# Optimization experiments

Hardware: AMD Instinct MI355X
Metric: run time of the kernel (lower is better)

## Reference

```python
import jax, jax.numpy as jnp
import numpy as np

DT = 0.05      # bsde.delta_t
EPS = 1e-6     # BatchNormalization epsilon


def _bn(x, gamma, beta):
    # training-mode batch norm: statistics over the batch axis
    m = jnp.mean(x, axis=0, keepdims=True)
    v = jnp.var(x, axis=0, keepdims=True)
    return (x - m) * jax.lax.rsqrt(v + EPS) * gamma + beta


def _subnet(x, g0, b0, W0, g1, b1, W1, g2, b2, W2, bias2, g3, b3):
    # bn -> (dense -> bn -> relu) x 2 -> dense(+bias) -> bn
    x = _bn(x, g0, b0)
    x = jax.nn.relu(_bn(x @ W0, g1, b1))
    x = jax.nn.relu(_bn(x @ W1, g2, b2))
    x = _bn(x @ W2 + bias2, g3, b3)
    return x


def setup_inputs() -> dict:
    key = jax.random.key(0)
    B, D, N, H = 8192, 100, 20, 110
    T = N - 1  # number of subnets
    ks = jax.random.split(key, 18)
    u = lambda k, s, lo, hi: jax.random.uniform(k, s, jnp.float32, lo, hi)
    s_dh = np.sqrt(2.0 / (D + H)).astype(np.float32)
    s_hh = np.sqrt(2.0 / (H + H)).astype(np.float32)
    s_hd = np.sqrt(2.0 / (H + D)).astype(np.float32)
    return {
        "dw": jax.random.normal(ks[0], (B, D, N), jnp.float32) * np.sqrt(DT).astype(np.float32),
        "x": jax.random.normal(ks[1], (B, D, N + 1), jnp.float32),
        "mean_y_input": jax.random.normal(ks[2], (N,), jnp.float32),
        "y_init": u(ks[3], (1,), 0.0, 1.0),
        "z_init": u(ks[4], (1, D), -0.1, 0.1),
        "gamma0": u(ks[5], (T, D), 0.1, 0.5),
        "beta0": 0.1 * jax.random.normal(ks[6], (T, D), jnp.float32),
        "W0": s_dh * jax.random.normal(ks[7], (T, D, H), jnp.float32),
        "gamma1": u(ks[8], (T, H), 0.1, 0.5),
        "beta1": 0.1 * jax.random.normal(ks[9], (T, H), jnp.float32),
        "W1": s_hh * jax.random.normal(ks[10], (T, H, H), jnp.float32),
        "gamma2": u(ks[11], (T, H), 0.1, 0.5),
        "beta2": 0.1 * jax.random.normal(ks[12], (T, H), jnp.float32),
        "W2": s_hd * jax.random.normal(ks[13], (T, H, D), jnp.float32),
        "bias2": jnp.zeros((T, D), jnp.float32),
        "gamma3": u(ks[14], (T, D), 0.1, 0.5),
        "beta3": 0.1 * jax.random.normal(ks[15], (T, D), jnp.float32),
    }


def reference(dw, x, mean_y_input, y_init, z_init, gamma0, beta0, W0,
              gamma1, beta1, W1, gamma2, beta2, W2, bias2, gamma3, beta3):
    B, D, N = dw.shape
    T = N - 1
    # z at step t+1 depends only on x[:, :, t+1] and subnet t -> compute all in parallel
    x_steps = jnp.moveaxis(x[:, :, 1:N], 2, 0)  # [T, B, D]
    z_all = jax.vmap(_subnet)(x_steps, gamma0, beta0, W0, gamma1, beta1, W1,
                              gamma2, beta2, W2, bias2, gamma3, beta3) / D  # [T, B, D]
    z0 = jnp.broadcast_to(z_init, (B, D))          # all_one_vec @ z_init
    zs = jnp.concatenate([z0[None], z_all], axis=0)  # [N, B, D] (z used at each update)
    dw_steps = jnp.moveaxis(dw, 2, 0)               # [N, B, D]
    y0 = jnp.ones((B, 1), dw.dtype) * y_init

    def step(y, zd):
        z, dwt = zd
        # f_tf(t, x, y, z) = sin(y) for the SineBM equation
        y_new = y - DT * jnp.sin(y) + jnp.sum(z * dwt, axis=1, keepdims=True)
        return y_new, jnp.mean(y_new)

    y_final, means = jax.lax.scan(step, y0, (zs, dw_steps))
    mean_y = jnp.concatenate([jnp.mean(y0)[None], means[:T]])  # length N
    return y_final, mean_y
```

## Files before the change

kernel.cpp:

```cpp
#include <hip/hip_runtime.h>

typedef unsigned short u16;
typedef unsigned int   u32;

#define BATCH  8192
#define DIM    100
#define HID    110
#define TSUB   19
#define NSTEP  20
#define KP     128
#define NPAD   112
#define BN_EPS 1e-6f
#define DT_C   0.05f

#define SAB  2048
#define SAR  (BATCH / SAB)
#define SLICES 32
#define NBLK_SCAN 2048
#define NMT  64

typedef __bf16 v8bf __attribute__((ext_vector_type(8)));
typedef float  v4f  __attribute__((ext_vector_type(4)));
typedef float  v2f  __attribute__((ext_vector_type(2)));
typedef u16    u16x4 __attribute__((ext_vector_type(4)));

__device__ __forceinline__ u16 f2bf(float f) {
    u32 u = __float_as_uint(f);
    return (u16)((u + 0x7fffu + ((u >> 16) & 1u)) >> 16);
}
__device__ __forceinline__ float bf2f(u16 h) {
    return __uint_as_float(((u32)h) << 16);
}
__device__ __forceinline__ void acc4(float4& s, float4& q, float4 v) {
    s.x += v.x; s.y += v.y; s.z += v.z; s.w += v.w;
    q.x += v.x * v.x; q.y += v.y * v.y; q.z += v.z * v.z; q.w += v.w * v.w;
}

__global__ void statsA(const float* __restrict__ x, float* __restrict__ part,
                       u32* __restrict__ xT32) {
    __shared__ u16 xls[SAR][2112];
    const int tid = threadIdx.x;
    const int b0 = blockIdx.x * SAR;
    float4 s0 = {0,0,0,0}, q0 = {0,0,0,0};
    float4 s1 = {0,0,0,0}, q1 = {0,0,0,0};
    float4 s2 = {0,0,0,0}, q2 = {0,0,0,0};
#pragma unroll
    for (int r = 0; r < SAR; r++) {
        const float4* row = (const float4*)(x + (size_t)(b0 + r) * 2100);
        float4 v0 = row[tid];
        float4 v1 = row[tid + 256];
        acc4(s0, q0, v0);
        acc4(s1, q1, v1);
        u16x4 p0 = { f2bf(v0.x), f2bf(v0.y), f2bf(v0.z), f2bf(v0.w) };
        u16x4 p1 = { f2bf(v1.x), f2bf(v1.y), f2bf(v1.z), f2bf(v1.w) };
        *(u16x4*)&xls[r][tid * 4]        = p0;
        *(u16x4*)&xls[r][1024 + tid * 4] = p1;
        if (tid < 13) {
            float4 v2 = row[tid + 512];
            acc4(s2, q2, v2);
            u16x4 p2 = { f2bf(v2.x), f2bf(v2.y), f2bf(v2.z), f2bf(v2.w) };
            *(u16x4*)&xls[r][2048 + tid * 4] = p2;
        }
    }
    float* ps = part + (size_t)blockIdx.x * 4200;
    *(float4*)&ps[tid * 4]               = s0;
    *(float4*)&ps[1024 + tid * 4]        = s1;
    *(float4*)&ps[2100 + tid * 4]        = q0;
    *(float4*)&ps[2100 + 1024 + tid * 4] = q1;
    if (tid < 13) {
        *(float4*)&ps[2048 + tid * 4]        = s2;
        *(float4*)&ps[2100 + 2048 + tid * 4] = q2;
    }
    __syncthreads();
    const int TOT = TSUB * SAR * (NPAD / 2);
    for (int i = tid; i < TOT; i += 256) {
        int w = i % (NPAD / 2);
        int seg = i / (NPAD / 2);
        int r = seg % SAR, t = seg / SAR;
        int d0 = w * 2;
        u32 v = 0;
        if (d0 < DIM) {
            u16 lo = xls[r][d0 * 21 + t + 1];
            u16 hi = (d0 + 1 < DIM) ? xls[r][(d0 + 1) * 21 + t + 1] : (u16)0;
            v = (u32)lo | ((u32)hi << 16);
        }
        xT32[((size_t)t * BATCH + b0 + r) * (NPAD / 2) + w] = v;
    }
}

__global__ void statsB(const float* __restrict__ part, float* __restrict__ slpart) {
    int gid = blockIdx.x * 256 + threadIdx.x;
    if (gid >= 4200 * SLICES) return;
    int slice = gid / 4200;
    int o = gid - slice * 4200;
    const float* p = part + (size_t)slice * (SAB / SLICES) * 4200 + o;
    float acc = 0.f;
#pragma unroll 8
    for (int i = 0; i < SAB / SLICES; i++) acc += p[(size_t)i * 4200];
    slpart[(size_t)slice * 4200 + o] = acc;
}

__global__ void statsC(const float* __restrict__ slpart, float* __restrict__ sum0) {
    int o = blockIdx.x * 256 + threadIdx.x;
    if (o >= 4200) return;
    float s = 0.f;
#pragma unroll
    for (int i = 0; i < SLICES; i++) s += slpart[(size_t)i * 4200 + o];
    sum0[o] = s;
}

__global__ void wtrans(const float* __restrict__ W0, const float* __restrict__ W1,
                       const float* __restrict__ W2, u16* __restrict__ WTsw) {
    __shared__ float lw[HID * HID];
    const int t = blockIdx.x, l = blockIdx.y, tid = threadIdx.x;
    const float* W; int K, N;
    if (l == 0)      { W = W0; K = DIM; N = HID; }
    else if (l == 1) { W = W1; K = HID; N = HID; }
    else             { W = W2; K = HID; N = DIM; }
    const float* Wt = W + (size_t)t * K * N;
    for (int i = tid; i < K * N; i += 256) lw[i] = Wt[i];
    __syncthreads();
    u16* out = WTsw + ((size_t)l * TSUB + t) * (NPAD * KP);
    for (int i = tid; i < NPAD * 16; i += 256) {
        int n = i / 16, p = i % 16;
        int kc = p ^ (n & 7);
        u16 o8[8];
#pragma unroll
        for (int j = 0; j < 8; j++) {
            int k = kc * 8 + j;
            float v = (k < K && n < N) ? lw[k * N + n] : 0.f;
            o8[j] = f2bf(v);
        }
        *(uint4*)&out[(size_t)n * KP + p * 8] = *(uint4*)o8;
    }
}

__global__ void scaleW0(const float* __restrict__ sum0, const float* __restrict__ sq0,
                        const float* __restrict__ g0, u16* __restrict__ WT0) {
    __shared__ float aL[DIM];
    const int t = blockIdx.x, tid = threadIdx.x;
    if (tid < DIM) {
        int idx = tid * 21 + (t + 1);
        float m = sum0[idx] * (1.f / BATCH);
        float v = sq0[idx] * (1.f / BATCH) - m * m;
        aL[tid] = g0[t * DIM + tid] * rsqrtf(v + BN_EPS);
    }
    __syncthreads();
    u16* wt = WT0 + (size_t)t * NPAD * KP;
    for (int i = tid; i < NPAD * 16; i += 256) {
        int n = i >> 4, p = i & 15;
        int kc = p ^ (n & 7);
        uint4 v4 = *(uint4*)&wt[(size_t)n * KP + p * 8];
        u16* e = (u16*)&v4;
#pragma unroll
        for (int j = 0; j < 8; j++) {
            int k = kc * 8 + j;
            if (k < DIM) e[j] = f2bf(bf2f(e[j]) * aL[k]);
        }
        *(uint4*)&wt[(size_t)n * KP + p * 8] = v4;
    }
}

template <int KREAL, int NOUT, int AFFINE, int RELU, int BMAJOR>
__global__ __launch_bounds__(512, 4)
void gemm_kernel(const u16* __restrict__ Ain,
                 const u16* __restrict__ WTswL,
                 const float* __restrict__ partIn,
                 const float* __restrict__ gIn,
                 const float* __restrict__ bIn,
                 u16* __restrict__ Hout,
                 float* __restrict__ partOut) {
    __shared__ __align__(16) u16 Blds[NPAD * KP];
    __shared__ float s_sum[NPAD], s_sq[NPAD];
    __shared__ float aAffL[KP], cAffL[KP];

    const int tid = threadIdx.x;
    const int mt = blockIdx.x;
    const int t  = blockIdx.y;
    const int brow0 = mt * 128;

    if (tid < NPAD) { s_sum[tid] = 0.f; s_sq[tid] = 0.f; }
    if (AFFINE) {
        if (tid >= KREAL && tid < KP) { aAffL[tid] = 0.f; cAffL[tid] = 0.f; }
        if (tid < KREAL) {
            float s = 0.f, q = 0.f;
#pragma unroll 8
            for (int m2 = 0; m2 < NMT; m2++) {
                const float* pp = partIn + ((size_t)(m2 * TSUB + t) * 2) * NPAD;
                s += pp[tid];
                q += pp[NPAD + tid];
            }
            float m = s * (1.f / BATCH);
            float v = q * (1.f / BATCH) - m * m;
            float rstd = rsqrtf(v + BN_EPS);
            int idx = t * KREAL + tid;
            float ga = gIn[idx] * rstd;
            aAffL[tid] = ga;
            cAffL[tid] = bIn[idx] - m * ga;
        }
    }

    {
        const uint4* wsrc = (const uint4*)(WTswL + (size_t)t * NPAD * KP);
        uint4* bl = (uint4*)Blds;
        for (int i = tid; i < NPAD * KP / 8; i += 512) bl[i] = wsrc[i];
    }
    __syncthreads();

    const int lane = tid & 63;
    const int wv   = tid >> 6;
    const int r0   = lane & 15;
    const int q    = lane >> 4;
    const int row  = wv * 16 + r0;

    const u16* arow = Ain + ((size_t)t * BATCH + brow0 + row) * NPAD;
    u16 hv[4][8];
#pragma unroll
    for (int ks = 0; ks < 4; ks++) {
        int cb = ks * 4 + q;
        int cbl = (cb > 13) ? 13 : cb;
        *(uint4*)hv[ks] = *(const uint4*)(arow + cbl * 8);
    }
    v8bf afr[4];
#pragma unroll
    for (int ks = 0; ks < 4; ks++) {
        if (AFFINE) {
            int cb = ks * 4 + q;
            const float* ap = &aAffL[cb * 8];
            const float* cp = &cAffL[cb * 8];
            u16 pk[8];
#pragma unroll
            for (int j = 0; j < 8; j++) {
                float av = fmaf(bf2f(hv[ks][j]), ap[j], cp[j]);
                if (RELU) av = fmaxf(av, 0.f);
                pk[j] = f2bf(av);
            }
            afr[ks] = *(v8bf*)pk;
        } else {
            afr[ks] = *(v8bf*)hv[ks];
        }
    }

    v4f acc[7];
#pragma unroll
    for (int j = 0; j < 7; j++) { v4f z = {0.f, 0.f, 0.f, 0.f}; acc[j] = z; }
#pragma unroll
    for (int ks = 0; ks < 4; ks++) {
        int cbase = ks * 4 + q;
#pragma unroll
        for (int nf = 0; nf < 7; nf++) {
            int nr = nf * 16 + r0;
            v8bf bfr = *(const v8bf*)&Blds[nr * KP + ((cbase ^ (nr & 7)) * 8)];
            acc[nf] = __builtin_amdgcn_mfma_f32_16x16x32_bf16(afr[ks], bfr, acc[nf], 0, 0, 0);
        }
    }

#pragma unroll
    for (int nf = 0; nf < 7; nf++) {
        int n = nf * 16 + r0;
#pragma unroll
        for (int rg = 0; rg < 4; rg++) {
            int grow = brow0 + wv * 16 + q * 4 + rg;
            size_t oidx = BMAJOR ? ((size_t)grow * (TSUB * NPAD) + (size_t)t * NPAD + n)
                                 : (((size_t)t * BATCH + grow) * NPAD + n);
            Hout[oidx] = f2bf(acc[nf][rg]);
        }
    }
#pragma unroll
    for (int nf = 0; nf < 7; nf++) {
        float cs = 0.f, cq = 0.f;
#pragma unroll
        for (int rg = 0; rg < 4; rg++) {
            float vv = acc[nf][rg];
            cs += vv; cq += vv * vv;
        }
        cs += __shfl_xor(cs, 16); cs += __shfl_xor(cs, 32);
        cq += __shfl_xor(cq, 16); cq += __shfl_xor(cq, 32);
        if (q == 0) {
            atomicAdd(&s_sum[nf * 16 + r0], cs);
            atomicAdd(&s_sq[nf * 16 + r0], cq);
        }
    }
    __syncthreads();
    if (tid < NPAD) {
        float* pp = partOut + ((size_t)(mt * TSUB + t) * 2) * NPAD;
        pp[tid]        = s_sum[tid];
        pp[NPAD + tid] = s_sq[tid];
    }
}

__global__ void finalize3(const float* __restrict__ partIn,
                          const float* __restrict__ g3, const float* __restrict__ b3,
                          float4* __restrict__ acg) {
    int i = blockIdx.x * 256 + threadIdx.x;
    if (i >= TSUB * 50) return;
    int t = i / 50, p = i - t * 50;
    float4 o;
#pragma unroll
    for (int h = 0; h < 2; h++) {
        int d = 2 * p + h;
        float s = 0.f, q = 0.f;
#pragma unroll 8
        for (int m2 = 0; m2 < NMT; m2++) {
            const float* pp = partIn + ((size_t)(m2 * TSUB + t) * 2) * NPAD;
            s += pp[d];
            q += pp[NPAD + d];
        }
        float m = s * (1.f / BATCH);
        float v = q * (1.f / BATCH) - m * m;
        float rstd = rsqrtf(v + BN_EPS);
        int e = t * DIM + d;
        float ga = g3[e] * rstd * (1.f / DIM);
        float cc = b3[e] * (1.f / DIM) - m * ga;
        if (h == 0) { o.x = ga; o.y = cc; } else { o.z = ga; o.w = cc; }
    }
    acg[i] = o;
}

__global__ __launch_bounds__(256, 4)
void scan_kernel(const float* __restrict__ dw,
                 const u16* __restrict__ zbuf,
                 const float4* __restrict__ acg,
                 const float* __restrict__ z_init, const float* __restrict__ y_init,
                 float* __restrict__ yout, float* __restrict__ mred) {
    __shared__ float bsum[NSTEP];
    const int tid = threadIdx.x;
    if (tid < NSTEP) bsum[tid] = 0.f;
    __syncthreads();

    const int wv = tid >> 6, lane = tid & 63;
    const int b = blockIdx.x * 4 + wv;
    const int ll = (lane < 50) ? lane : 49;

    v4f w[10];
    u32 zr[TSUB];
    v2f zi;
    {
        const float* dwaddr = dw + (size_t)b * (DIM * NSTEP) + ll * 40;
        const u16*   zaddr  = zbuf + (size_t)b * (TSUB * NPAD) + 2 * ll;
        const float* ziaddr = z_init + 2 * ll;
        asm volatile("global_load_dwordx4 %0, %1, off offset:0"   : "=v"(w[0]) : "v"(dwaddr));
        asm volatile("global_load_dwordx4 %0, %1, off offset:16"  : "=v"(w[1]) : "v"(dwaddr));
        asm volatile("global_load_dwordx4 %0, %1, off offset:32"  : "=v"(w[2]) : "v"(dwaddr));
        asm volatile("global_load_dwordx4 %0, %1, off offset:48"  : "=v"(w[3]) : "v"(dwaddr));
        asm volatile("global_load_dwordx4 %0, %1, off offset:64"  : "=v"(w[4]) : "v"(dwaddr));
        asm volatile("global_load_dwordx4 %0, %1, off offset:80"  : "=v"(w[5]) : "v"(dwaddr));
        asm volatile("global_load_dwordx4 %0, %1, off offset:96"  : "=v"(w[6]) : "v"(dwaddr));
        asm volatile("global_load_dwordx4 %0, %1, off offset:112" : "=v"(w[7]) : "v"(dwaddr));
        asm volatile("global_load_dwordx4 %0, %1, off offset:128" : "=v"(w[8]) : "v"(dwaddr));
        asm volatile("global_load_dwordx4 %0, %1, off offset:144" : "=v"(w[9]) : "v"(dwaddr));
#pragma unroll
        for (int t = 0; t < TSUB; t++)
            asm volatile("global_load_dword %0, %1, off offset:%2"
                         : "=v"(zr[t]) : "v"(zaddr), "i"(t * NPAD * 2));
        asm volatile("global_load_dwordx2 %0, %1, off" : "=v"(zi) : "v"(ziaddr));
        asm volatile("s_waitcnt vmcnt(0)" ::: "memory");
        __builtin_amdgcn_sched_barrier(0);
    }

    float acc[NSTEP];
#pragma unroll
    for (int k = 0; k < NSTEP; k++) acc[k] = 0.f;
    if (lane < 50) {
        acc[0] = zi[0] * w[0][0] + zi[1] * w[5][0];
#pragma unroll
        for (int t = 0; t < TSUB; t++) {
            float4 ac = acg[t * 50 + ll];
            u32 z = zr[t];
            float za0 = fmaf(bf2f((u16)(z & 0xffffu)), ac.x, ac.y);
            float za1 = fmaf(bf2f((u16)(z >> 16)),     ac.z, ac.w);
            const int n = t + 1, j = n >> 2, k = n & 3;
            acc[n] += w[j][k] * za0 + w[5 + j][k] * za1;
        }
    }

#pragma unroll
    for (int m = 1; m < 64; m <<= 1) {
#pragma unroll
        for (int k = 0; k < NSTEP; k++) acc[k] += __shfl_xor(acc[k], m, 64);
    }

    const float yi = y_init[0];
    float y = yi, ysave = 0.f;
#pragma unroll
    for (int i = 0; i < NSTEP; i++) {
        y = y - DT_C * __sinf(y) + acc[i];
        if (i == lane - 1) ysave = y;
    }
    if (lane == 0) yout[b] = y;
    if (lane >= 1 && lane < NSTEP) atomicAdd(&bsum[lane], ysave);
    __syncthreads();
    if (tid >= 1 && tid < NSTEP) mred[blockIdx.x * NSTEP + tid] = bsum[tid];
}

__global__ void meanred(const float* __restrict__ mred, const float* __restrict__ y_init,
                        float* __restrict__ meanout) {
    const int n = blockIdx.x, tid = threadIdx.x;
    if (n == 0) { if (tid == 0) meanout[0] = y_init[0]; return; }
    float s = 0.f;
    for (int i = tid; i < NBLK_SCAN; i += 256) s += mred[(size_t)i * NSTEP + n];
#pragma unroll
    for (int m = 1; m < 64; m <<= 1) s += __shfl_xor(s, m, 64);
    __shared__ float ws4[4];
    if ((tid & 63) == 0) ws4[tid >> 6] = s;
    __syncthreads();
    if (tid == 0) meanout[n] = (ws4[0] + ws4[1] + ws4[2] + ws4[3]) * (1.f / BATCH);
}

extern "C" void kernel_launch(void* const* d_in, const int* in_sizes, int n_in,
                              void* d_out, int out_size, void* d_ws, size_t ws_size,
                              hipStream_t stream) {
    const float* dw     = (const float*)d_in[0];
    const float* x      = (const float*)d_in[1];
    const float* y_init = (const float*)d_in[3];
    const float* z_init = (const float*)d_in[4];
    const float* g0 = (const float*)d_in[5];
    const float* W0 = (const float*)d_in[7];
    const float* g1 = (const float*)d_in[8];
    const float* b1 = (const float*)d_in[9];
    const float* W1 = (const float*)d_in[10];
    const float* g2 = (const float*)d_in[11];
    const float* b2 = (const float*)d_in[12];
    const float* W2 = (const float*)d_in[13];
    const float* g3 = (const float*)d_in[15];
    const float* b3 = (const float*)d_in[16];

    char* ws = (char*)d_ws;
    size_t off = 0;
    auto alloc = [&](size_t bytes) -> void* {
        off = (off + 255) & ~(size_t)255;
        void* p = ws + off;
        off += bytes;
        return p;
    };

    float* sum0   = (float*)alloc(4200 * 4);
    float* slpart = (float*)alloc((size_t)SLICES * 4200 * 4);
    float* gp0    = (float*)alloc((size_t)NMT * TSUB * 2 * NPAD * 4);
    float* gp1    = (float*)alloc((size_t)NMT * TSUB * 2 * NPAD * 4);

    u16* WTsw = (u16*)alloc((size_t)3 * TSUB * NPAD * KP * 2);
    float4* acg = (float4*)alloc((size_t)TSUB * 50 * 16);
    float* mred = (float*)alloc((size_t)NBLK_SCAN * NSTEP * 4);

    const size_t hBytes = (size_t)TSUB * BATCH * NPAD * 2;
    u16* h0 = (u16*)alloc(hBytes);
    u16* h1 = (u16*)alloc(hBytes);
    u16* outbuf = h0;
    float* part = (float*)h0;
    u32*  xT32  = (u32*)h1;

    float* yout = (float*)d_out;
    float* meanout = yout + BATCH;

    wtrans<<<dim3(TSUB, 3), 256, 0, stream>>>(W0, W1, W2, WTsw);
    statsA<<<SAB, 256, 0, stream>>>(x, part, xT32);
    statsB<<<(4200 * SLICES + 255) / 256, 256, 0, stream>>>(part, slpart);
    statsC<<<(4200 + 255) / 256, 256, 0, stream>>>(slpart, sum0);

    const u16* xT = (const u16*)xT32;
    u16* WT0 = WTsw;
    u16* WT1 = WTsw + (size_t)TSUB * NPAD * KP;
    u16* WT2 = WTsw + (size_t)2 * TSUB * NPAD * KP;

    scaleW0<<<TSUB, 256, 0, stream>>>(sum0, sum0 + 2100, g0, WT0);

    gemm_kernel<DIM, HID, 0, 0, 0><<<dim3(NMT, TSUB), 512, 0, stream>>>(xT, WT0, nullptr, nullptr, nullptr, h0, gp0);
    gemm_kernel<HID, HID, 1, 1, 0><<<dim3(NMT, TSUB), 512, 0, stream>>>(h0, WT1, gp0, g1, b1, h1, gp1);
    gemm_kernel<HID, DIM, 1, 1, 1><<<dim3(NMT, TSUB), 512, 0, stream>>>(h1, WT2, gp1, g2, b2, outbuf, gp0);

    finalize3<<<4, 256, 0, stream>>>(gp0, g3, b3, acg);
    scan_kernel<<<NBLK_SCAN, 256, 0, stream>>>(dw, outbuf, acg, z_init, y_init, yout, mred);
    meanred<<<NSTEP, 256, 0, stream>>>(mred, y_init, meanout);
}
```

Before: 172.0 us.

## Fold first-layer batch-norm scaling into GEMM prologue and drop statsC/scaleW0

Removes the statsC reduction kernel and the scaleW0 weight-rescaling kernel. The first GEMM now reduces the 32 slice partials itself and applies the per-feature scale to the activations in its prologue (affine mode 2, no shift). statsA is also restructured to issue all row loads before computing, with launch bounds set for more memory-level parallelism. This cuts two launches and their serialization, at the cost of every GEMM block redundantly reducing the slice partials. The activation is now scaled before bf16 rounding rather than the weights, which slightly changes rounding.

Measured after the change: 179.0 us. +4.1%, slower.

```diff
diff --git a/kernel.cpp b/kernel.cpp
--- a/kernel.cpp
+++ b/kernel.cpp
@@ -36,29 +36,40 @@
     q.x += v.x * v.x; q.y += v.y * v.y; q.z += v.z * v.z; q.w += v.w * v.w;
 }
 
-__global__ void statsA(const float* __restrict__ x, float* __restrict__ part,
-                       u32* __restrict__ xT32) {
+__global__ __launch_bounds__(256, 4)
+void statsA(const float* __restrict__ x, float* __restrict__ part,
+            u32* __restrict__ xT32) {
     __shared__ u16 xls[SAR][2112];
     const int tid = threadIdx.x;
     const int b0 = blockIdx.x * SAR;
+
+    const float4* rp[SAR];
+#pragma unroll
+    for (int r = 0; r < SAR; r++)
+        rp[r] = (const float4*)(x + (size_t)(b0 + r) * 2100);
+    float4 va[SAR], vb[SAR], vc[SAR];
+    const int tt = (tid < 13) ? tid : 12;
+#pragma unroll
+    for (int r = 0; r < SAR; r++) va[r] = rp[r][tid];
+#pragma unroll
+    for (int r = 0; r < SAR; r++) vb[r] = rp[r][tid + 256];
+#pragma unroll
+    for (int r = 0; r < SAR; r++) vc[r] = rp[r][tt + 512];
+
     float4 s0 = {0,0,0,0}, q0 = {0,0,0,0};
     float4 s1 = {0,0,0,0}, q1 = {0,0,0,0};
     float4 s2 = {0,0,0,0}, q2 = {0,0,0,0};
 #pragma unroll
     for (int r = 0; r < SAR; r++) {
-        const float4* row = (const float4*)(x + (size_t)(b0 + r) * 2100);
-        float4 v0 = row[tid];
-        float4 v1 = row[tid + 256];
-        acc4(s0, q0, v0);
-        acc4(s1, q1, v1);
-        u16x4 p0 = { f2bf(v0.x), f2bf(v0.y), f2bf(v0.z), f2bf(v0.w) };
-        u16x4 p1 = { f2bf(v1.x), f2bf(v1.y), f2bf(v1.z), f2bf(v1.w) };
+        acc4(s0, q0, va[r]);
+        acc4(s1, q1, vb[r]);
+        u16x4 p0 = { f2bf(va[r].x), f2bf(va[r].y), f2bf(va[r].z), f2bf(va[r].w) };
+        u16x4 p1 = { f2bf(vb[r].x), f2bf(vb[r].y), f2bf(vb[r].z), f2bf(vb[r].w) };
         *(u16x4*)&xls[r][tid * 4]        = p0;
         *(u16x4*)&xls[r][1024 + tid * 4] = p1;
         if (tid < 13) {
-            float4 v2 = row[tid + 512];
-            acc4(s2, q2, v2);
-            u16x4 p2 = { f2bf(v2.x), f2bf(v2.y), f2bf(v2.z), f2bf(v2.w) };
+            acc4(s2, q2, vc[r]);
+            u16x4 p2 = { f2bf(vc[r].x), f2bf(vc[r].y), f2bf(vc[r].z), f2bf(vc[r].w) };
             *(u16x4*)&xls[r][2048 + tid * 4] = p2;
         }
     }
@@ -100,15 +111,6 @@
     slpart[(size_t)slice * 4200 + o] = acc;
 }
 
-__global__ void statsC(const float* __restrict__ slpart, float* __restrict__ sum0) {
-    int o = blockIdx.x * 256 + threadIdx.x;
-    if (o >= 4200) return;
-    float s = 0.f;
-#pragma unroll
-    for (int i = 0; i < SLICES; i++) s += slpart[(size_t)i * 4200 + o];
-    sum0[o] = s;
-}
-
 __global__ void wtrans(const float* __restrict__ W0, const float* __restrict__ W1,
                        const float* __restrict__ W2, u16* __restrict__ WTsw) {
     __shared__ float lw[HID * HID];
@@ -135,33 +137,7 @@
     }
 }
 
-__global__ void scaleW0(const float* __restrict__ sum0, const float* __restrict__ sq0,
-                        const float* __restrict__ g0, u16* __restrict__ WT0) {
-    __shared__ float aL[DIM];
-    const int t = blockIdx.x, tid = threadIdx.x;
-    if (tid < DIM) {
-        int idx = tid * 21 + (t + 1);
-        float m = sum0[idx] * (1.f / BATCH);
-        float v = sq0[idx] * (1.f / BATCH) - m * m;
-        aL[tid] = g0[t * DIM + tid] * rsqrtf(v + BN_EPS);
-    }
-    __syncthreads();
-    u16* wt = WT0 + (size_t)t * NPAD * KP;
-    for (int i = tid; i < NPAD * 16; i += 256) {
-        int n = i >> 4, p = i & 15;
-        int kc = p ^ (n & 7);
-        uint4 v4 = *(uint4*)&wt[(size_t)n * KP + p * 8];
-        u16* e = (u16*)&v4;
-#pragma unroll
-        for (int j = 0; j < 8; j++) {
-            int k = kc * 8 + j;
-            if (k < DIM) e[j] = f2bf(bf2f(e[j]) * aL[k]);
-        }
-        *(uint4*)&wt[(size_t)n * KP + p * 8] = v4;
-    }
-}
-
-template <int KREAL, int NOUT, int AFFINE, int RELU, int BMAJOR>
+template <int KREAL, int NOUT, int AFFMODE, int RELU, int BMAJOR>
 __global__ __launch_bounds__(512, 4)
 void gemm_kernel(const u16* __restrict__ Ain,
                  const u16* __restrict__ WTswL,
@@ -180,23 +156,31 @@
     const int brow0 = mt * 128;
 
     if (tid < NPAD) { s_sum[tid] = 0.f; s_sq[tid] = 0.f; }
-    if (AFFINE) {
+    if (AFFMODE) {
         if (tid >= KREAL && tid < KP) { aAffL[tid] = 0.f; cAffL[tid] = 0.f; }
         if (tid < KREAL) {
             float s = 0.f, q = 0.f;
+            if (AFFMODE == 1) {
 #pragma unroll 8
-            for (int m2 = 0; m2 < NMT; m2++) {
-                const float* pp = partIn + ((size_t)(m2 * TSUB + t) * 2) * NPAD;
-                s += pp[tid];
-                q += pp[NPAD + tid];
+                for (int m2 = 0; m2 < NMT; m2++) {
+                    const float* pp = partIn + ((size_t)(m2 * TSUB + t) * 2) * NPAD;
+                    s += pp[tid];
+                    q += pp[NPAD + tid];
+                }
+            } else {
+                int idx = tid * 21 + (t + 1);
+#pragma unroll 8
+                for (int s2 = 0; s2 < SLICES; s2++) {
+                    s += partIn[(size_t)s2 * 4200 + idx];
+                    q += partIn[(size_t)s2 * 4200 + 2100 + idx];
+                }
             }
             float m = s * (1.f / BATCH);
             float v = q * (1.f / BATCH) - m * m;
             float rstd = rsqrtf(v + BN_EPS);
-            int idx = t * KREAL + tid;
-            float ga = gIn[idx] * rstd;
+            float ga = gIn[t * KREAL + tid] * rstd;
             aAffL[tid] = ga;
-            cAffL[tid] = bIn[idx] - m * ga;
+            cAffL[tid] = (AFFMODE == 2) ? 0.f : (bIn[t * KREAL + tid] - m * ga);
         }
     }
 
@@ -224,7 +208,7 @@
     v8bf afr[4];
 #pragma unroll
     for (int ks = 0; ks < 4; ks++) {
-        if (AFFINE) {
+        if (AFFMODE) {
             int cb = ks * 4 + q;
             const float* ap = &aAffL[cb * 8];
             const float* cp = &cAffL[cb * 8];
@@ -434,7 +418,6 @@
         return p;
     };
 
-    float* sum0   = (float*)alloc(4200 * 4);
     float* slpart = (float*)alloc((size_t)SLICES * 4200 * 4);
     float* gp0    = (float*)alloc((size_t)NMT * TSUB * 2 * NPAD * 4);
     float* gp1    = (float*)alloc((size_t)NMT * TSUB * 2 * NPAD * 4);
@@ -456,16 +439,13 @@
     wtrans<<<dim3(TSUB, 3), 256, 0, stream>>>(W0, W1, W2, WTsw);
     statsA<<<SAB, 256, 0, stream>>>(x, part, xT32);
     statsB<<<(4200 * SLICES + 255) / 256, 256, 0, stream>>>(part, slpart);
-    statsC<<<(4200 + 255) / 256, 256, 0, stream>>>(slpart, sum0);
 
     const u16* xT = (const u16*)xT32;
     u16* WT0 = WTsw;
     u16* WT1 = WTsw + (size_t)TSUB * NPAD * KP;
     u16* WT2 = WTsw + (size_t)2 * TSUB * NPAD * KP;
 
-    scaleW0<<<TSUB, 256, 0, stream>>>(sum0, sum0 + 2100, g0, WT0);
-
-    gemm_kernel<DIM, HID, 0, 0, 0><<<dim3(NMT, TSUB), 512, 0, stream>>>(xT, WT0, nullptr, nullptr, nullptr, h0, gp0);
+    gemm_kernel<DIM, HID, 2, 0, 0><<<dim3(NMT, TSUB), 512, 0, stream>>>(xT, WT0, slpart, g0, nullptr, h0, gp0);
     gemm_kernel<HID, HID, 1, 1, 0><<<dim3(NMT, TSUB), 512, 0, stream>>>(h0, WT1, gp0, g1, b1, h1, gp1);
     gemm_kernel<HID, DIM, 1, 1, 1><<<dim3(NMT, TSUB), 512, 0, stream>>>(h1, WT2, gp1, g2, b2, outbuf, gp0);
 
```
